# Kernel tuning notes

Hardware: AMD Instinct MI355X
Metric: run time of the kernel (lower is better)

## Reference

```python
import jax, jax.numpy as jnp
import numpy as np
import itertools

# --- static config (matches init_kwargs) ---
RX, RZ = 32, 16          # input resolutions
RX_, RZ_ = 16, 8         # subsampled resolutions
STRIDE, T = 2, 1         # stride, template_number
B, C = 32, 256           # batch, in_dim
H, KD, AR = 8, 64, 2     # num_heads, key_dim, attn_ratio
D = AR * KD              # per-head v dim = 128
DH = D * H               # 1024
NHKD = KD * H            # 512
OUT = 384                # out_dim
N = RX * RX + T * RZ * RZ    # 1280
N_ = RX_ * RX_ + T * RZ_ * RZ_  # 320
EPS = 1e-5


def _bias_idxs():
    pts = list(itertools.product(range(RX), range(RX)))
    for i in range(T):
        pts += list(itertools.product(range(RX + RZ * i, RX + RZ * (i + 1)),
                                      range(RX + RZ * i, RX + RZ * (i + 1))))
    pts_ = list(itertools.product(range(RX_), range(RX_)))
    for i in range(T):
        pts_ += list(itertools.product(range(RX_ + RZ_ * i, RX_ + RZ_ * (i + 1)),
                                       range(RX_ + RZ_ * i, RX_ + RZ_ * (i + 1))))
    p = np.asarray(pts)    # [N,2]
    p_ = np.asarray(pts_)  # [N_,2]
    off = np.abs(p_[:, None, :] * STRIDE - p[None, :, :]).reshape(-1, 2)
    uniq, inv = np.unique(off, axis=0, return_inverse=True)
    return inv.reshape(len(pts_), len(pts)).astype(np.int32), len(uniq)


def _linear_bn(x, W, g, b, rm, rv):
    # Linear (no bias) followed by eval-mode BatchNorm1d over channels.
    y = jnp.einsum('bnc,hc->bnh', x, W)
    return (y - rm) * (g * jax.lax.rsqrt(rv + EPS)) + b


def _subsample(x):
    # x: [B, N, C] -> [B, N_, C], strided 2D subsampling of each block.
    Bx = x.shape[0]
    xz = x[:, :RX * RX].reshape(Bx, RX, RX, C)[:, ::STRIDE, ::STRIDE].reshape(Bx, -1, C)
    outs = [xz]
    for i in range(T):
        s = RX * RX + i * RZ * RZ
        z = x[:, s:s + RZ * RZ].reshape(Bx, RZ, RZ, C)[:, ::STRIDE, ::STRIDE].reshape(Bx, -1, C)
        outs.append(z)
    return jnp.concatenate(outs, axis=1)


def setup_inputs() -> dict:
    key = jax.random.key(0)
    ks = jax.random.split(key, 12)
    idxs_np, n_off = _bias_idxs()
    HKV = DH + NHKD  # 1536

    def bn(k, dim):
        k1, k2, k3, k4 = jax.random.split(k, 4)
        return (jax.random.normal(k1, (dim,)) * 0.1 + 1.0,   # gamma
                jax.random.normal(k2, (dim,)) * 0.1,          # beta
                jax.random.normal(k3, (dim,)) * 0.1,          # running_mean
                jax.random.uniform(k4, (dim,)) * 0.5 + 0.5)   # running_var

    g_kv, b_kv, rm_kv, rv_kv = bn(ks[1], HKV)
    g_q, b_q, rm_q, rv_q = bn(ks[3], NHKD)
    g_p, b_p, rm_p, rv_p = bn(ks[5], OUT)
    return {
        'x': jax.random.normal(ks[0], (B, N, C), dtype=jnp.float32),
        'W_kv': jax.random.normal(ks[6], (HKV, C)) * (C ** -0.5),
        'g_kv': g_kv, 'b_kv': b_kv, 'rm_kv': rm_kv, 'rv_kv': rv_kv,
        'W_q': jax.random.normal(ks[7], (NHKD, C)) * (C ** -0.5),
        'g_q': g_q, 'b_q': b_q, 'rm_q': rm_q, 'rv_q': rv_q,
        'W_p': jax.random.normal(ks[8], (OUT, DH)) * (DH ** -0.5),
        'g_p': g_p, 'b_p': b_p, 'rm_p': rm_p, 'rv_p': rv_p,
        'attn_bias': jax.random.normal(ks[9], (H, n_off)) * 0.02,
        'bias_idxs': jnp.asarray(idxs_np),
    }


def reference(x, W_kv, g_kv, b_kv, rm_kv, rv_kv,
              W_q, g_q, b_q, rm_q, rv_q,
              W_p, g_p, b_p, rm_p, rv_p,
              attn_bias, bias_idxs):
    Bx = x.shape[0]
    scale = KD ** -0.5
    # kv branch: [B,N,H*(KD+D)]
    kv = _linear_bn(x, W_kv, g_kv, b_kv, rm_kv, rv_kv).reshape(Bx, N, H, KD + D)
    k = kv[..., :KD].transpose(0, 2, 1, 3)   # [B,H,N,KD]
    v = kv[..., KD:].transpose(0, 2, 1, 3)   # [B,H,N,D]
    # q branch: subsample then project
    q = _linear_bn(_subsample(x), W_q, g_q, b_q, rm_q, rv_q)
    q = q.reshape(Bx, N_, H, KD).transpose(0, 2, 1, 3)  # [B,H,N_,KD]
    # scores + gathered relative position bias
    bias = attn_bias[:, bias_idxs]                       # [H,N_,N]
    attn = jnp.einsum('bhqd,bhkd->bhqk', q, k) * scale + bias
    attn = jax.nn.softmax(attn, axis=-1)
    o = jnp.einsum('bhqk,bhkd->bhqd', attn, v)           # [B,H,N_,D]
    o = o.transpose(0, 2, 1, 3).reshape(Bx, N_, DH)
    # proj: Hardswish then Linear_BN
    o = jax.nn.hard_swish(o)
    return _linear_bn(o, W_p, g_p, b_p, rm_p, rv_p)      # [B,N_,OUT]
```

## Files before the change

### kernel.cpp

```cpp
#include <hip/hip_runtime.h>
#include <hip/hip_bf16.h>
#include <cstdint>
#include <cstddef>

typedef unsigned short u16;
typedef __bf16 bf16x8 __attribute__((ext_vector_type(8)));
typedef float  f32x4  __attribute__((ext_vector_type(4)));
typedef u16    u16x8  __attribute__((ext_vector_type(8)));
typedef u16    u16x4  __attribute__((ext_vector_type(4)));
typedef short  s16x4  __attribute__((ext_vector_type(4)));

#define MFMA16(A_, B_, C_) __builtin_amdgcn_mfma_f32_16x16x32_bf16((A_), (B_), (C_), 0, 0, 0)
#define MFMA16K16(A_, B_, C_) __builtin_amdgcn_mfma_f32_16x16x16bf16_1k((A_), (B_), (C_), 0, 0, 0)

#define LOG2E 1.4426950408889634f

#if __has_builtin(__builtin_amdgcn_exp2f)
#define EXP2(x) __builtin_amdgcn_exp2f(x)
#else
#define EXP2(x) exp2f(x)
#endif

__device__ __forceinline__ u16 f2bf(float f) {
  return __builtin_bit_cast(u16, (__bf16)f);
}
__device__ __forceinline__ float bf2f(u16 v) {
  return (float)__builtin_bit_cast(__bf16, v);
}

__device__ __forceinline__ void async16(u16* lds, const u16* g) {
  __builtin_amdgcn_global_load_lds(
      (const __attribute__((address_space(1))) unsigned int*)g,
      (__attribute__((address_space(3))) unsigned int*)lds, 16, 0, 0);
}


__global__ void cvt_f32_bf16(const float* __restrict__ src, u16* __restrict__ dst, int n4) {
  int i = blockIdx.x * 256 + threadIdx.x;
  if (i < n4) {
    const float4 v = ((const float4*)src)[i];
    u16x4 o;
    o[0] = f2bf(v.x); o[1] = f2bf(v.y); o[2] = f2bf(v.z); o[3] = f2bf(v.w);
    ((u16x4*)dst)[i] = o;
  }
}

__device__ __forceinline__ void cvt4(const float* src, u16* dst, int i) {
  const float4 v = ((const float4*)src)[i];
  u16x4 o;
  o[0] = f2bf(v.x); o[1] = f2bf(v.y); o[2] = f2bf(v.z); o[3] = f2bf(v.w);
  ((u16x4*)dst)[i] = o;
}

__device__ __forceinline__ void bn1(const float* g, const float* b, const float* rm,
                                    const float* rv, float* alpha, float* beta,
                                    int i, float scale) {
  float a0 = g[i] * rsqrtf(rv[i] + 1e-5f);
  alpha[i] = a0 * scale;
  beta[i]  = (b[i] - rm[i] * a0) * scale;
}

__global__ void prep_fused(
    const float* __restrict__ Wkv, const float* __restrict__ Wq, const float* __restrict__ Wp,
    u16* __restrict__ wkv_bf, u16* __restrict__ wq_bf, u16* __restrict__ wp_bf,
    const float* __restrict__ g_kv, const float* __restrict__ b_kv,
    const float* __restrict__ rm_kv, const float* __restrict__ rv_kv,
    float* __restrict__ al_kv, float* __restrict__ be_kv,
    const float* __restrict__ g_q, const float* __restrict__ b_q,
    const float* __restrict__ rm_q, const float* __restrict__ rv_q,
    float* __restrict__ al_q, float* __restrict__ be_q,
    const float* __restrict__ g_p, const float* __restrict__ b_p,
    const float* __restrict__ rm_p, const float* __restrict__ rv_p,
    float* __restrict__ al_p, float* __restrict__ be_p) {
  const int bid = blockIdx.x, t = threadIdx.x;
  if (bid < 384) {
    cvt4(Wkv, wkv_bf, bid * 256 + t);
  } else if (bid < 512) {
    cvt4(Wq, wq_bf, (bid - 384) * 256 + t);
  } else if (bid < 896) {
    cvt4(Wp, wp_bf, (bid - 512) * 256 + t);
  } else if (bid < 902) {
    bn1(g_kv, b_kv, rm_kv, rv_kv, al_kv, be_kv, (bid - 896) * 256 + t, 1.0f);
  } else if (bid < 904) {
    bn1(g_q, b_q, rm_q, rv_q, al_q, be_q, (bid - 902) * 256 + t, 0.125f * LOG2E);
  } else {
    const int i = (bid - 904) * 256 + t;
    if (i < 384) bn1(g_p, b_p, rm_p, rv_p, al_p, be_p, i, 1.0f);
  }
}

__global__ void bias_expand_frag(const float* __restrict__ attn_bias, const int* __restrict__ idxs,
                                 u16* __restrict__ bias_frag, int n_off) {
  int i = blockIdx.x * 256 + threadIdx.x;
  if (i >= 8 * 5 * 40 * 256 * 8) return;
  const int e8  = i & 7;
  const int nn  = e8 >> 2;
  const int j   = e8 & 3;
  const int tid = (i >> 3) & 255;
  int v = i >> 11;
  const int kt = v % 40; v /= 40;
  const int qt = v % 5;
  const int h  = v / 5;
  const int w = tid >> 6, lr = (tid >> 4) & 3, lc = tid & 15;
  const int q = qt * 64 + w * 16 + lc;
  const int k = kt * 32 + nn * 16 + lr * 4 + j;
  bias_frag[i] = f2bf(attn_bias[h * n_off + idxs[q * 1280 + k]] * LOG2E);
}


__global__ __launch_bounds__(256) void gemm_kv(
    const u16* __restrict__ A, const u16* __restrict__ Wt,
    const float* __restrict__ alpha, const float* __restrict__ beta,
    u16* __restrict__ k_buf, u16* __restrict__ vt_buf) {
  __shared__ __align__(16) u16 As[128 * 64];
  __shared__ __align__(16) u16 Bs[128 * 64];
  const int tid  = threadIdx.x;
  const int lane = tid & 63;
  const int w    = tid >> 6;
  const int wr   = (w >> 1) * 64, wc = (w & 1) * 64;
  const int lr   = lane >> 4, lc = lane & 15;
  const int m0   = blockIdx.x * 128;
  const int n0   = blockIdx.y * 128;
  const int scol  = (lane & 7) * 8;
  f32x4 acc[4][4] = {};

  for (int kt = 0; kt < 256; kt += 64) {
    if (kt) __syncthreads();
#pragma unroll
    for (int i = 0; i < 4; ++i) {
      const int row = w * 32 + i * 8 + (lane >> 3);
      async16(&As[(w * 32 + i * 8) * 64], A  + (size_t)(m0 + row) * 256 + kt + scol);
      async16(&Bs[(w * 32 + i * 8) * 64], Wt + (size_t)(n0 + row) * 256 + kt + scol);
    }
    __syncthreads();
#pragma unroll
    for (int kk = 0; kk < 2; ++kk) {
      bf16x8 af[4], bff[4];
#pragma unroll
      for (int m = 0; m < 4; ++m)
        af[m] = *(const bf16x8*)(&As[(wr + m * 16 + lc) * 64 + kk * 32 + lr * 8]);
#pragma unroll
      for (int n = 0; n < 4; ++n)
        bff[n] = *(const bf16x8*)(&Bs[(wc + n * 16 + lc) * 64 + kk * 32 + lr * 8]);
#pragma unroll
      for (int m = 0; m < 4; ++m)
#pragma unroll
        for (int n = 0; n < 4; ++n)
          acc[m][n] = MFMA16(af[m], bff[n], acc[m][n]);
    }
  }

  const int jr = lr * 4;
#pragma unroll
  for (int m = 0; m < 4; ++m) {
    const int r0  = m0 + wr + m * 16 + jr;
    const int b   = r0 / 1280;
    const int np0 = r0 - b * 1280;
    const int kt  = np0 >> 5;
    const int kl  = np0 & 31;
#pragma unroll
    for (int n = 0; n < 4; ++n) {
      const int c    = n0 + wc + n * 16 + lc;
      const float al = alpha[c], be = beta[c];
      const int head = c / 192;
      const int off  = c - head * 192;
      const size_t bh = (size_t)(b * 8 + head);
      if (off < 64) {
        const size_t base = ((bh * 40 + kt) << 11);
#pragma unroll
        for (int j = 0; j < 4; ++j) {
          const int r = kl + j;
          k_buf[base + (r << 6) + ((((off >> 3) ^ (r & 7)) << 3)) + (off & 7)] =
              f2bf(acc[m][n][j] * al + be);
        }
      } else {
        const int d = off - 64;
        u16x4 pk;
#pragma unroll
        for (int j = 0; j < 4; ++j) pk[j] = f2bf(acc[m][n][j] * al + be);
        const size_t dst = ((size_t)(bh * 40 + kt) << 12) + d * 32 +
                           ((((kl >> 2) + (d >> 1)) & 7) << 2);
        *(u16x4*)(&vt_buf[dst]) = pk;
      }
    }
  }
}


__device__ __forceinline__ int sub_src_row(int qr) {
  if (qr < 256) return ((qr >> 4) * 64) + ((qr & 15) * 2);
  int rr = qr - 256;
  return 1024 + ((rr >> 3) * 32) + ((rr & 7) * 2);
}

__global__ __launch_bounds__(256) void gemm_q(
    const u16* __restrict__ X, const u16* __restrict__ Wt,
    const float* __restrict__ alpha, const float* __restrict__ beta,
    u16* __restrict__ q_buf) {
  __shared__ __align__(16) u16 As[128 * 64];
  __shared__ __align__(16) u16 Bs[128 * 64];
  const int tid  = threadIdx.x;
  const int lane = tid & 63;
  const int w    = tid >> 6;
  const int wr   = (w >> 1) * 64, wc = (w & 1) * 64;
  const int lr   = lane >> 4, lc = lane & 15;
  const int m0   = blockIdx.x * 128;
  const int n0   = blockIdx.y * 128;
  const int scol  = (lane & 7) * 8;
  f32x4 acc[4][4] = {};

  for (int kt = 0; kt < 256; kt += 64) {
    if (kt) __syncthreads();
#pragma unroll
    for (int i = 0; i < 4; ++i) {
      const int row = w * 32 + i * 8 + (lane >> 3);
      const int gr  = m0 + row;
      const int bb  = gr / 320;
      const int qr  = gr - bb * 320;
      async16(&As[(w * 32 + i * 8) * 64],
              X + (size_t)(bb * 1280 + sub_src_row(qr)) * 256 + kt + scol);
      async16(&Bs[(w * 32 + i * 8) * 64], Wt + (size_t)(n0 + row) * 256 + kt + scol);
    }
    __syncthreads();
#pragma unroll
    for (int kk = 0; kk < 2; ++kk) {
      bf16x8 af[4], bff[4];
#pragma unroll
      for (int m = 0; m < 4; ++m)
        af[m] = *(const bf16x8*)(&As[(wr + m * 16 + lc) * 64 + kk * 32 + lr * 8]);
#pragma unroll
      for (int n = 0; n < 4; ++n)
        bff[n] = *(const bf16x8*)(&Bs[(wc + n * 16 + lc) * 64 + kk * 32 + lr * 8]);
#pragma unroll
      for (int m = 0; m < 4; ++m)
#pragma unroll
        for (int n = 0; n < 4; ++n)
          acc[m][n] = MFMA16(af[m], bff[n], acc[m][n]);
    }
  }

  const int jr = lr * 4;
#pragma unroll
  for (int m = 0; m < 4; ++m) {
#pragma unroll
    for (int n = 0; n < 4; ++n) {
      const int c    = n0 + wc + n * 16 + lc;
      const float al = alpha[c], be = beta[c];
      const int head = c >> 6, kd = c & 63;
#pragma unroll
      for (int j = 0; j < 4; ++j) {
        const int r  = m0 + wr + m * 16 + jr + j;
        const int b  = r / 320;
        const int qr = r - b * 320;
        q_buf[((size_t)(b * 8 + head) * 320 + qr) * 64 + kd] = f2bf(acc[m][n][j] * al + be);
      }
    }
  }
}


__global__ __launch_bounds__(256) void attn_kernel(
    const u16* __restrict__ q_buf, const u16* __restrict__ kphys,
    const u16* __restrict__ vphys, const u16* __restrict__ bias_frag,
    u16* __restrict__ o_buf) {
  __shared__ __align__(16) u16 Kb[2][2048];
  __shared__ __align__(16) u16 Vb[2][4096];
  const int tid  = threadIdx.x;
  const int lane = tid & 63;
  const int w    = tid >> 6;
  const int lr   = lane >> 4, lc = lane & 15, jr = lr * 4;
  const int g   = blockIdx.x;
  const int f   = (g & 7) * 160 + (g >> 3);
  const int qt  = f % 5;
  const int bh_ = f / 5;
  const int h = bh_ & 7, b = bh_ >> 3;
  const size_t bh = (size_t)bh_;
  const int q0 = qt * 64 + w * 16;

  bf16x8 bq0, bq1;
  {
    const u16* qp = q_buf + (bh * 320 + q0 + lc) * 64 + lr * 8;
    bq0 = *(const bf16x8*)(qp);
    bq1 = *(const bf16x8*)(qp + 32);
  }

  f32x4 oacc[8] = {};
  float lacc = 0.f;

  const u16* kt_base   = kphys + bh * (40 * 2048);
  const u16* vt_base   = vphys + bh * (40 * 4096);
  const u16* bias_base = bias_frag + (((size_t)(h * 5 + qt) * 40) * 256 + tid) * 8;

  const int ko0 = lc * 64 + ((lr ^ (lc & 7)) << 3);
  const int ko1 = lc * 64 + (((4 + lr) ^ (lc & 7)) << 3);
  const int po0 = lc * 32 + ((lr + (lc >> 1)) & 7) * 4;
  const int po1 = lc * 32 + ((4 + lr + (lc >> 1)) & 7) * 4;

  u16x8 bbA, bbB;

  auto issue = [&](int buf, int kt) {
    async16(&Kb[buf][w * 512], kt_base + kt * 2048 + w * 512 + lane * 8);
    const u16* vs = vt_base + kt * 4096 + (w * 2) * 512 + lane * 8;
    async16(&Vb[buf][(w * 2) * 512], vs);
    async16(&Vb[buf][(w * 2 + 1) * 512], vs + 512);
  };
  auto gbias = [&](int kt, u16x8* dst) {
    *dst = *(const u16x8*)(bias_base + (size_t)kt * 2048);
  };

  auto compute = [&](int buf, const u16x8* bb) {
    const u16* Ksb = Kb[buf];
    const u16* Vsb = Vb[buf];
    const u16* bptr = (const u16*)bb;

    f32x4 s[2];
    __builtin_amdgcn_s_setprio(1);
#pragma unroll
    for (int n = 0; n < 2; ++n) {
      const bf16x8 kf0 = *(const bf16x8*)(Ksb + n * 1024 + ko0);
      const bf16x8 kf1 = *(const bf16x8*)(Ksb + n * 1024 + ko1);
      f32x4 t;
#pragma unroll
      for (int j = 0; j < 4; ++j) t[j] = bf2f(bptr[n * 4 + j]);
      t = MFMA16(kf0, bq0, t);
      t = MFMA16(kf1, bq1, t);
      s[n] = t;
    }
    __builtin_amdgcn_s_setprio(0);

    s16x4 pa[2];
    float ssum = 0.f;
#pragma unroll
    for (int n = 0; n < 2; ++n) {
      u16x4 pk;
#pragma unroll
      for (int j = 0; j < 4; ++j) {
        const float e = EXP2(s[n][j]);
        ssum += e;
        pk[j] = f2bf(e);
      }
      pa[n] = __builtin_bit_cast(s16x4, pk);
    }
    lacc += ssum;

    __builtin_amdgcn_s_setprio(1);
#pragma unroll
    for (int nc = 0; nc < 8; ++nc) {
      const u16* vrow = Vsb + nc * 512;
      const s16x4 vf0 = __builtin_bit_cast(s16x4, *(const u16x4*)(vrow + po0));
      const s16x4 vf1 = __builtin_bit_cast(s16x4, *(const u16x4*)(vrow + po1));
      oacc[nc] = MFMA16K16(pa[0], vf0, oacc[nc]);
      oacc[nc] = MFMA16K16(pa[1], vf1, oacc[nc]);
    }
    __builtin_amdgcn_s_setprio(0);
  };

#define WAITBAR(N)                                                       \
  asm volatile("s_waitcnt vmcnt(" #N ") lgkmcnt(0)" ::: "memory");       \
  __builtin_amdgcn_s_barrier();

  issue(0, 0);
  gbias(0, &bbA);
  WAITBAR(1)

#pragma unroll 1
  for (int t = 0; t < 40; t += 2) {
    issue(1, t + 1);
    gbias(t + 1, &bbB);
    compute(0, &bbA);
    WAITBAR(1)
    if (t + 2 < 40) { issue(0, t + 2); gbias(t + 2, &bbA); }
    compute(1, &bbB);
    WAITBAR(1)
  }
#undef WAITBAR

  lacc += __shfl_xor(lacc, 16);
  lacc += __shfl_xor(lacc, 32);
  float invl[4];
#pragma unroll
  for (int j = 0; j < 4; ++j) invl[j] = 1.f / __shfl(lacc, jr + j);

#pragma unroll
  for (int nc = 0; nc < 8; ++nc)
#pragma unroll
    for (int j = 0; j < 4; ++j) {
      const float xv = oacc[nc][j] * invl[j];
      const float hs = xv * fminf(fmaxf(xv + 3.f, 0.f), 6.f) * (1.f / 6.f);
      o_buf[((size_t)b * 320 + q0 + jr + j) * 1024 + h * 128 + nc * 16 + lc] = f2bf(hs);
    }
}


__global__ __launch_bounds__(256) void gemm_p(
    const u16* __restrict__ O, const u16* __restrict__ Wt,
    const float* __restrict__ alpha, const float* __restrict__ beta,
    float* __restrict__ out) {
  __shared__ __align__(16) u16 As[128 * 64];
  __shared__ __align__(16) u16 Bs[128 * 64];
  const int tid  = threadIdx.x;
  const int lane = tid & 63;
  const int w    = tid >> 6;
  const int wr   = (w >> 1) * 64, wc = (w & 1) * 64;
  const int lr   = lane >> 4, lc = lane & 15;
  const int m0   = blockIdx.x * 128;
  const int n0   = blockIdx.y * 128;
  const int scol  = (lane & 7) * 8;
  f32x4 acc[4][4] = {};

  for (int kt = 0; kt < 1024; kt += 64) {
    if (kt) __syncthreads();
#pragma unroll
    for (int i = 0; i < 4; ++i) {
      const int row = w * 32 + i * 8 + (lane >> 3);
      async16(&As[(w * 32 + i * 8) * 64], O  + (size_t)(m0 + row) * 1024 + kt + scol);
      async16(&Bs[(w * 32 + i * 8) * 64], Wt + (size_t)(n0 + row) * 1024 + kt + scol);
    }
    __syncthreads();
#pragma unroll
    for (int kk = 0; kk < 2; ++kk) {
      bf16x8 af[4], bff[4];
#pragma unroll
      for (int m = 0; m < 4; ++m)
        af[m] = *(const bf16x8*)(&As[(wr + m * 16 + lc) * 64 + kk * 32 + lr * 8]);
#pragma unroll
      for (int n = 0; n < 4; ++n)
        bff[n] = *(const bf16x8*)(&Bs[(wc + n * 16 + lc) * 64 + kk * 32 + lr * 8]);
#pragma unroll
      for (int m = 0; m < 4; ++m)
#pragma unroll
        for (int n = 0; n < 4; ++n)
          acc[m][n] = MFMA16(af[m], bff[n], acc[m][n]);
    }
  }

  const int jr = lr * 4;
#pragma unroll
  for (int m = 0; m < 4; ++m) {
#pragma unroll
    for (int n = 0; n < 4; ++n) {
      const int c = n0 + wc + n * 16 + lc;
      const float al = alpha[c], be = beta[c];
#pragma unroll
      for (int j = 0; j < 4; ++j) {
        const int r = m0 + wr + m * 16 + jr + j;
        out[(size_t)r * 384 + c] = acc[m][n][j] * al + be;
      }
    }
  }
}


extern "C" void kernel_launch(void* const* d_in, const int* in_sizes, int n_in,
                              void* d_out, int out_size, void* d_ws, size_t ws_size,
                              hipStream_t stream) {
  const float* x      = (const float*)d_in[0];
  const float* W_kv   = (const float*)d_in[1];
  const float* g_kv   = (const float*)d_in[2];
  const float* b_kv   = (const float*)d_in[3];
  const float* rm_kv  = (const float*)d_in[4];
  const float* rv_kv  = (const float*)d_in[5];
  const float* W_q    = (const float*)d_in[6];
  const float* g_q    = (const float*)d_in[7];
  const float* b_q    = (const float*)d_in[8];
  const float* rm_q   = (const float*)d_in[9];
  const float* rv_q   = (const float*)d_in[10];
  const float* W_p    = (const float*)d_in[11];
  const float* g_p    = (const float*)d_in[12];
  const float* b_p    = (const float*)d_in[13];
  const float* rm_p   = (const float*)d_in[14];
  const float* rv_p   = (const float*)d_in[15];
  const float* attn_bias = (const float*)d_in[16];
  const int*   bias_idxs = (const int*)d_in[17];
  const int n_off = in_sizes[16] / 8;

  char* ws = (char*)d_ws;
  size_t off = 0;
  auto alloc = [&](size_t bytes) -> void* {
    void* p = ws + off;
    off += (bytes + 255) & ~(size_t)255;
    return p;
  };
  u16* x_bf    = (u16*)alloc((size_t)40960 * 256 * 2);
  u16* wkv_bf  = (u16*)alloc((size_t)1536 * 256 * 2);
  u16* wq_bf   = (u16*)alloc((size_t)512 * 256 * 2);
  u16* wp_bf   = (u16*)alloc((size_t)384 * 1024 * 2);
  float* al_kv = (float*)alloc(1536 * 4);
  float* be_kv = (float*)alloc(1536 * 4);
  float* al_q  = (float*)alloc(512 * 4);
  float* be_q  = (float*)alloc(512 * 4);
  float* al_p  = (float*)alloc(384 * 4);
  float* be_p  = (float*)alloc(384 * 4);
  u16* k_buf   = (u16*)alloc((size_t)256 * 40 * 2048 * 2);
  u16* vt_buf  = (u16*)alloc((size_t)256 * 40 * 4096 * 2);
  u16* q_buf   = (u16*)alloc((size_t)32 * 8 * 320 * 64 * 2);
  u16* bias_fr = (u16*)alloc((size_t)8 * 5 * 40 * 256 * 8 * 2);
  u16* o_buf   = (u16*)alloc((size_t)32 * 320 * 1024 * 2);
  (void)ws_size; (void)n_in; (void)out_size;

  cvt_f32_bf16<<<(2621440 + 255) / 256, 256, 0, stream>>>(x, x_bf, 2621440);
  prep_fused<<<906, 256, 0, stream>>>(
      W_kv, W_q, W_p, wkv_bf, wq_bf, wp_bf,
      g_kv, b_kv, rm_kv, rv_kv, al_kv, be_kv,
      g_q, b_q, rm_q, rv_q, al_q, be_q,
      g_p, b_p, rm_p, rv_p, al_p, be_p);
  bias_expand_frag<<<(3276800 + 255) / 256, 256, 0, stream>>>(attn_bias, bias_idxs, bias_fr, n_off);

  gemm_kv<<<dim3(320, 12), 256, 0, stream>>>(x_bf, wkv_bf, al_kv, be_kv, k_buf, vt_buf);
  gemm_q<<<dim3(80, 4), 256, 0, stream>>>(x_bf, wq_bf, al_q, be_q, q_buf);
  attn_kernel<<<dim3(1280), 256, 0, stream>>>(q_buf, k_buf, vt_buf, bias_fr, o_buf);
  gemm_p<<<dim3(80, 3), 256, 0, stream>>>(o_buf, wp_bf, al_p, be_p, (float*)d_out);
}
```

Baseline: 193.6 us.

## Merge prep kernels and KV/Q GEMMs, stage KV epilogue through LDS

Combines the x conversion, weight conversion, BN folding and bias fragment expansion into one launch, and merges the KV and Q projection GEMMs into a single grid that picks its role by block index. The KV epilogue now writes the swizzled K and transposed V tiles into shared memory first, then copies them out with coalesced 16-byte stores instead of scattered 2- and 8-byte global writes. This aims to cut launch overhead and uncoalesced write traffic, at the cost of an extra LDS round trip with two barriers and the assumption that each 128-row tile stays within one batch and 64-column groups line up with K/V boundaries.

```diff
diff --git a/kernel.cpp b/kernel.cpp
--- a/kernel.cpp
+++ b/kernel.cpp
@@ -35,16 +35,6 @@
 }
 
 
-__global__ void cvt_f32_bf16(const float* __restrict__ src, u16* __restrict__ dst, int n4) {
-  int i = blockIdx.x * 256 + threadIdx.x;
-  if (i < n4) {
-    const float4 v = ((const float4*)src)[i];
-    u16x4 o;
-    o[0] = f2bf(v.x); o[1] = f2bf(v.y); o[2] = f2bf(v.z); o[3] = f2bf(v.w);
-    ((u16x4*)dst)[i] = o;
-  }
-}
-
 __device__ __forceinline__ void cvt4(const float* src, u16* dst, int i) {
   const float4 v = ((const float4*)src)[i];
   u16x4 o;
@@ -60,7 +50,8 @@
   beta[i]  = (b[i] - rm[i] * a0) * scale;
 }
 
-__global__ void prep_fused(
+__global__ void prep_all(
+    const float* __restrict__ x, u16* __restrict__ x_bf,
     const float* __restrict__ Wkv, const float* __restrict__ Wq, const float* __restrict__ Wp,
     u16* __restrict__ wkv_bf, u16* __restrict__ wq_bf, u16* __restrict__ wp_bf,
     const float* __restrict__ g_kv, const float* __restrict__ b_kv,
@@ -71,56 +62,59 @@
     float* __restrict__ al_q, float* __restrict__ be_q,
     const float* __restrict__ g_p, const float* __restrict__ b_p,
     const float* __restrict__ rm_p, const float* __restrict__ rv_p,
-    float* __restrict__ al_p, float* __restrict__ be_p) {
+    float* __restrict__ al_p, float* __restrict__ be_p,
+    const float* __restrict__ attn_bias, const int* __restrict__ idxs,
+    u16* __restrict__ bias_frag, int n_off) {
   const int bid = blockIdx.x, t = threadIdx.x;
-  if (bid < 384) {
-    cvt4(Wkv, wkv_bf, bid * 256 + t);
-  } else if (bid < 512) {
-    cvt4(Wq, wq_bf, (bid - 384) * 256 + t);
-  } else if (bid < 896) {
-    cvt4(Wp, wp_bf, (bid - 512) * 256 + t);
-  } else if (bid < 902) {
-    bn1(g_kv, b_kv, rm_kv, rv_kv, al_kv, be_kv, (bid - 896) * 256 + t, 1.0f);
-  } else if (bid < 904) {
-    bn1(g_q, b_q, rm_q, rv_q, al_q, be_q, (bid - 902) * 256 + t, 0.125f * LOG2E);
+  if (bid < 10240) {
+    cvt4(x, x_bf, bid * 256 + t);
+  } else if (bid < 10624) {
+    cvt4(Wkv, wkv_bf, (bid - 10240) * 256 + t);
+  } else if (bid < 10752) {
+    cvt4(Wq, wq_bf, (bid - 10624) * 256 + t);
+  } else if (bid < 11136) {
+    cvt4(Wp, wp_bf, (bid - 10752) * 256 + t);
+  } else if (bid < 11142) {
+    bn1(g_kv, b_kv, rm_kv, rv_kv, al_kv, be_kv, (bid - 11136) * 256 + t, 1.0f);
+  } else if (bid < 11144) {
+    bn1(g_q, b_q, rm_q, rv_q, al_q, be_q, (bid - 11142) * 256 + t, 0.125f * LOG2E);
+  } else if (bid < 11146) {
+    const int i = (bid - 11144) * 256 + t;
+    if (i < 384) bn1(g_p, b_p, rm_p, rv_p, al_p, be_p, i, 1.0f);
   } else {
-    const int i = (bid - 904) * 256 + t;
-    if (i < 384) bn1(g_p, b_p, rm_p, rv_p, al_p, be_p, i, 1.0f);
-  }
-}
-
-__global__ void bias_expand_frag(const float* __restrict__ attn_bias, const int* __restrict__ idxs,
-                                 u16* __restrict__ bias_frag, int n_off) {
-  int i = blockIdx.x * 256 + threadIdx.x;
-  if (i >= 8 * 5 * 40 * 256 * 8) return;
-  const int e8  = i & 7;
-  const int nn  = e8 >> 2;
-  const int j   = e8 & 3;
-  const int tid = (i >> 3) & 255;
-  int v = i >> 11;
-  const int kt = v % 40; v /= 40;
-  const int qt = v % 5;
-  const int h  = v / 5;
-  const int w = tid >> 6, lr = (tid >> 4) & 3, lc = tid & 15;
-  const int q = qt * 64 + w * 16 + lc;
-  const int k = kt * 32 + nn * 16 + lr * 4 + j;
-  bias_frag[i] = f2bf(attn_bias[h * n_off + idxs[q * 1280 + k]] * LOG2E);
-}
-
-
-__global__ __launch_bounds__(256) void gemm_kv(
+    int i = (bid - 11146) * 256 + t;
+    if (i < 8 * 5 * 40 * 256 * 8) {
+      const int e8  = i & 7;
+      const int nn  = e8 >> 2;
+      const int j   = e8 & 3;
+      const int tid = (i >> 3) & 255;
+      int v = i >> 11;
+      const int kt = v % 40; v /= 40;
+      const int qt = v % 5;
+      const int h  = v / 5;
+      const int w = tid >> 6, lr = (tid >> 4) & 3, lc = tid & 15;
+      const int q = qt * 64 + w * 16 + lc;
+      const int k = kt * 32 + nn * 16 + lr * 4 + j;
+      bias_frag[i] = f2bf(attn_bias[h * n_off + idxs[q * 1280 + k]] * LOG2E);
+    }
+  }
+}
+
+
+__device__ __forceinline__ void gemm_kv_part(
+    u16* S, int bid,
     const u16* __restrict__ A, const u16* __restrict__ Wt,
     const float* __restrict__ alpha, const float* __restrict__ beta,
     u16* __restrict__ k_buf, u16* __restrict__ vt_buf) {
-  __shared__ __align__(16) u16 As[128 * 64];
-  __shared__ __align__(16) u16 Bs[128 * 64];
+  u16* As = S;
+  u16* Bs = S + 8192;
   const int tid  = threadIdx.x;
   const int lane = tid & 63;
   const int w    = tid >> 6;
   const int wr   = (w >> 1) * 64, wc = (w & 1) * 64;
   const int lr   = lane >> 4, lc = lane & 15;
-  const int m0   = blockIdx.x * 128;
-  const int n0   = blockIdx.y * 128;
+  const int m0   = (bid % 320) * 128;
+  const int n0   = (bid / 320) * 128;
   const int scol  = (lane & 7) * 8;
   f32x4 acc[4][4] = {};
 
@@ -150,42 +144,67 @@
     }
   }
 
-  const int jr = lr * 4;
+  __syncthreads();
+  const int jr   = lr * 4;
+  const int b    = m0 / 1280;
+  const int np0  = m0 - b * 1280;
+  const int kt0  = np0 >> 5;
+  const int hh   = w & 1;
+  const int c0   = n0 + hh * 64;
+  const int head = c0 / 192;
+  const int rem  = c0 - head * 192;
+  u16* R = S + hh * 8192;
+  (void)head;
+
 #pragma unroll
   for (int m = 0; m < 4; ++m) {
-    const int r0  = m0 + wr + m * 16 + jr;
-    const int b   = r0 / 1280;
-    const int np0 = r0 - b * 1280;
-    const int kt  = np0 >> 5;
-    const int kl  = np0 & 31;
+    const int lrow = (w >> 1) * 64 + m * 16 + jr;
+    const int ktl  = lrow >> 5;
+    const int kl   = lrow & 31;
 #pragma unroll
     for (int n = 0; n < 4; ++n) {
-      const int c    = n0 + wc + n * 16 + lc;
+      const int ch = n * 16 + lc;
+      const int c  = c0 + ch;
       const float al = alpha[c], be = beta[c];
-      const int head = c / 192;
-      const int off  = c - head * 192;
-      const size_t bh = (size_t)(b * 8 + head);
-      if (off < 64) {
-        const size_t base = ((bh * 40 + kt) << 11);
+      if (rem == 0) {
 #pragma unroll
         for (int j = 0; j < 4; ++j) {
           const int r = kl + j;
-          k_buf[base + (r << 6) + ((((off >> 3) ^ (r & 7)) << 3)) + (off & 7)] =
+          R[ktl * 2048 + (r << 6) + (((ch >> 3) ^ (r & 7)) << 3) + (ch & 7)] =
               f2bf(acc[m][n][j] * al + be);
         }
       } else {
-        const int d = off - 64;
+        const int d = (rem - 64) + ch;
         u16x4 pk;
 #pragma unroll
         for (int j = 0; j < 4; ++j) pk[j] = f2bf(acc[m][n][j] * al + be);
-        const size_t dst = ((size_t)(bh * 40 + kt) << 12) + d * 32 +
-                           ((((kl >> 2) + (d >> 1)) & 7) << 2);
-        *(u16x4*)(&vt_buf[dst]) = pk;
+        *(u16x4*)(&R[ktl * 2048 + ch * 32 + ((((kl >> 2) + (d >> 1)) & 7) << 2)]) = pk;
       }
     }
   }
-}
-
+  __syncthreads();
+
+#pragma unroll
+  for (int g2 = 0; g2 < 2; ++g2) {
+    const int c0g  = n0 + g2 * 64;
+    const int hd   = c0g / 192;
+    const int remg = c0g - hd * 192;
+    const size_t bhg = (size_t)(b * 8 + hd);
+    const u16* Rg = S + g2 * 8192;
+    if (remg == 0) {
+      u16* dst = k_buf + ((bhg * 40 + kt0) << 11);
+#pragma unroll
+      for (int i = 0; i < 4; ++i)
+        *(u16x8*)(dst + i * 2048 + tid * 8) = *(const u16x8*)(Rg + i * 2048 + tid * 8);
+    } else {
+      const int dbase = remg - 64;
+#pragma unroll
+      for (int i = 0; i < 4; ++i)
+        *(u16x8*)(vt_buf + ((bhg * 40 + kt0 + i) << 12) + dbase * 32 + tid * 8) =
+            *(const u16x8*)(Rg + i * 2048 + tid * 8);
+    }
+  }
+}
 
 __device__ __forceinline__ int sub_src_row(int qr) {
   if (qr < 256) return ((qr >> 4) * 64) + ((qr & 15) * 2);
@@ -193,19 +212,20 @@
   return 1024 + ((rr >> 3) * 32) + ((rr & 7) * 2);
 }
 
-__global__ __launch_bounds__(256) void gemm_q(
+__device__ __forceinline__ void gemm_q_part(
+    u16* S, int id2,
     const u16* __restrict__ X, const u16* __restrict__ Wt,
     const float* __restrict__ alpha, const float* __restrict__ beta,
     u16* __restrict__ q_buf) {
-  __shared__ __align__(16) u16 As[128 * 64];
-  __shared__ __align__(16) u16 Bs[128 * 64];
+  u16* As = S;
+  u16* Bs = S + 8192;
   const int tid  = threadIdx.x;
   const int lane = tid & 63;
   const int w    = tid >> 6;
   const int wr   = (w >> 1) * 64, wc = (w & 1) * 64;
   const int lr   = lane >> 4, lc = lane & 15;
-  const int m0   = blockIdx.x * 128;
-  const int n0   = blockIdx.y * 128;
+  const int m0   = (id2 % 80) * 128;
+  const int n0   = (id2 / 80) * 128;
   const int scol  = (lane & 7) * 8;
   f32x4 acc[4][4] = {};
 
@@ -255,6 +275,22 @@
         q_buf[((size_t)(b * 8 + head) * 320 + qr) * 64 + kd] = f2bf(acc[m][n][j] * al + be);
       }
     }
+  }
+}
+
+__global__ __launch_bounds__(256) void gemm_kvq(
+    const u16* __restrict__ A, const u16* __restrict__ Wkv,
+    const float* __restrict__ al_kv, const float* __restrict__ be_kv,
+    u16* __restrict__ k_buf, u16* __restrict__ vt_buf,
+    const u16* __restrict__ Wq,
+    const float* __restrict__ al_q, const float* __restrict__ be_q,
+    u16* __restrict__ q_buf) {
+  __shared__ __align__(16) u16 S[16384];
+  const int bid = blockIdx.x;
+  if (bid < 3840) {
+    gemm_kv_part(S, bid, A, Wkv, al_kv, be_kv, k_buf, vt_buf);
+  } else {
+    gemm_q_part(S, bid - 3840, A, Wq, al_q, be_q, q_buf);
   }
 }
 
@@ -498,16 +534,17 @@
   u16* o_buf   = (u16*)alloc((size_t)32 * 320 * 1024 * 2);
   (void)ws_size; (void)n_in; (void)out_size;
 
-  cvt_f32_bf16<<<(2621440 + 255) / 256, 256, 0, stream>>>(x, x_bf, 2621440);
-  prep_fused<<<906, 256, 0, stream>>>(
-      W_kv, W_q, W_p, wkv_bf, wq_bf, wp_bf,
+  prep_all<<<23946, 256, 0, stream>>>(
+      x, x_bf, W_kv, W_q, W_p, wkv_bf, wq_bf, wp_bf,
       g_kv, b_kv, rm_kv, rv_kv, al_kv, be_kv,
       g_q, b_q, rm_q, rv_q, al_q, be_q,
-      g_p, b_p, rm_p, rv_p, al_p, be_p);
-  bias_expand_frag<<<(3276800 + 255) / 256, 256, 0, stream>>>(attn_bias, bias_idxs, bias_fr, n_off);
-
-  gemm_kv<<<dim3(320, 12), 256, 0, stream>>>(x_bf, wkv_bf, al_kv, be_kv, k_buf, vt_buf);
-  gemm_q<<<dim3(80, 4), 256, 0, stream>>>(x_bf, wq_bf, al_q, be_q, q_buf);
+      g_p, b_p, rm_p, rv_p, al_p, be_p,
+      attn_bias, bias_idxs, bias_fr, n_off);
+
+  gemm_kvq<<<4160, 256, 0, stream>>>(
+      x_bf, wkv_bf, al_kv, be_kv, k_buf, vt_buf,
+      wq_bf, al_q, be_q, q_buf);
+
   attn_kernel<<<dim3(1280), 256, 0, stream>>>(q_buf, k_buf, vt_buf, bias_fr, o_buf);
   gemm_p<<<dim3(80, 3), 256, 0, stream>>>(o_buf, wp_bf, al_p, be_p, (float*)d_out);
 }
```

Result: faster. 182.9 us (-5.5%).
